# Performance work log

Hardware: AMD Instinct MI355X
Metric: run time of the kernel (lower is better)

## Reference

```python
import jax, jax.numpy as jnp
import numpy as np

N_NODES = 65536


def gcn_conv(x, W, b, src, dst, n_nodes):
    """PyG GCNConv: symmetric-normalized aggregation with self-loops.
    out = D^{-1/2} (A + I) D^{-1/2} (x W) + b, deg counted on targets incl. self-loop.
    """
    h = x @ W  # [N, F_out]
    # in-degree including the self-loop
    deg = jnp.zeros((n_nodes,), dtype=x.dtype).at[dst].add(1.0) + 1.0
    dis = jax.lax.rsqrt(deg)  # deg^{-1/2}
    norm = dis[src] * dis[dst]  # [E]
    msg = h[src] * norm[:, None]  # [E, F_out] gathered+scaled messages
    agg = jax.ops.segment_sum(msg, dst, num_segments=n_nodes)
    agg = agg + h * (dis * dis)[:, None]  # self-loop contribution, norm = dis[i]^2
    return agg + b


def setup_inputs() -> dict:
    key = jax.random.key(0)
    k1, k2, k3, k4 = jax.random.split(key, 4)
    d_in, d_hid = 64, 64
    x = jax.random.normal(k1, (N_NODES, d_in), dtype=jnp.float32)
    edge_index = jax.random.randint(k2, (2, 1048576), 0, N_NODES, dtype=jnp.int64)
    s = 1.0 / np.sqrt(d_in)
    W1 = jax.random.normal(k3, (d_in, d_hid), dtype=jnp.float32) * s
    b1 = jnp.zeros((d_hid,), dtype=jnp.float32)
    W2 = jax.random.normal(k4, (d_hid, d_hid), dtype=jnp.float32) * s
    b2 = jnp.zeros((d_hid,), dtype=jnp.float32)
    return {"x": x, "edge_index": edge_index, "W1": W1, "b1": b1, "W2": W2, "b2": b2}


def reference(x, edge_index, W1, b1, W2, b2):
    src, dst = edge_index[0], edge_index[1]
    n = x.shape[0]
    h = jax.nn.relu(gcn_conv(x, W1, b1, src, dst, n))
    h = jax.nn.relu(gcn_conv(h, W2, b2, src, dst, n))
    return h
```

## Files before the change

kernel.cpp:

```cpp
#include <hip/hip_runtime.h>

#define FDIM 64
#define EPB  2048
#define BCAP 6144

typedef float nf4 __attribute__((ext_vector_type(4)));
typedef float nf2 __attribute__((ext_vector_type(2)));

__device__ __forceinline__ unsigned f2bf(float f) {
    unsigned u = __float_as_uint(f);
    u += 0x7fffu + ((u >> 16) & 1u);
    return u >> 16;
}
__device__ __forceinline__ float bflo(unsigned u) { return __uint_as_float(u << 16); }
__device__ __forceinline__ float bfhi(unsigned u) { return __uint_as_float(u & 0xffff0000u); }


__global__ __launch_bounds__(256) void k_coarse(const int* __restrict__ ei,
                                                int* __restrict__ cursorG,
                                                int* __restrict__ packed, int nE) {
    __shared__ int lh[256], gb[256], lc[256];
    int t = threadIdx.x;
    lh[t] = 0; lc[t] = 0;
    __syncthreads();
    int base = blockIdx.x * EPB;
    int bins[EPB / 256], vals[EPB / 256];
    #pragma unroll
    for (int i = 0; i < EPB / 256; ++i) {
        int e = base + i * 256 + t;
        if (e < nE) {
            int s = ei[e];
            int d = ei[nE + e];
            bins[i] = d >> 8;
            vals[i] = (s << 8) | (d & 255);
            atomicAdd(&lh[bins[i]], 1);
        } else {
            bins[i] = -1;
        }
    }
    __syncthreads();
    gb[t] = atomicAdd(&cursorG[t], lh[t]);
    __syncthreads();
    #pragma unroll
    for (int i = 0; i < EPB / 256; ++i) {
        int b = bins[i];
        if (b >= 0) {
            int p = gb[b] + atomicAdd(&lc[b], 1);
            if (p < BCAP) packed[b * BCAP + p] = vals[i];
        }
    }
}


__global__ __launch_bounds__(256) void k_fine(const int* __restrict__ packed,
                                              const int* __restrict__ cursorG,
                                              float* __restrict__ dis,
                                              int* __restrict__ rowStart,
                                              unsigned short* __restrict__ lenArr,
                                              unsigned short* __restrict__ sortedSrc,
                                              int n) {
    __shared__ int cnt[256], loc[256], lc[256];
    int t = threadIdx.x;
    int b = blockIdx.x;
    int lo = b * BCAP;
    int hi = lo + cursorG[b];
    cnt[t] = 0; lc[t] = 0;
    __syncthreads();
    for (int k = lo + t; k < hi; k += 256)
        atomicAdd(&cnt[packed[k] & 255], 1);
    __syncthreads();

    int c = cnt[t];
    int node = (b << 8) + t;
    dis[node]    = rsqrtf((float)c + 1.0f);
    lenArr[node] = (unsigned short)c;

    loc[t] = c;
    __syncthreads();
    #pragma unroll
    for (int off = 1; off < 256; off <<= 1) {
        int u = (t >= off) ? loc[t - off] : 0;
        __syncthreads();
        loc[t] += u;
        __syncthreads();
    }
    int excl = loc[t] - c;
    rowStart[node] = lo + excl;
    __syncthreads();
    loc[t] = excl;
    __syncthreads();

    for (int k = lo + t; k < hi; k += 256) {
        int v = packed[k];
        int dl = v & 255;
        int p = loc[dl] + atomicAdd(&lc[dl], 1);
        sortedSrc[lo + p] = (unsigned short)(v >> 8);
    }
}


__global__ __launch_bounds__(256) void k_gemm64s(const float* __restrict__ X,
                                                 const float* __restrict__ W,
                                                 const float* __restrict__ dis,
                                                 unsigned* __restrict__ Hb) {
    __shared__ float Ws[64 * 64];
    __shared__ float XsT[64 * 68];

    const int tid  = threadIdx.x;
    const int row0 = blockIdx.x * 64;

    for (int i = tid; i < 4096; i += 256) Ws[i] = W[i];
    for (int i = tid; i < 4096; i += 256) {
        int r = i >> 6, k = i & 63;
        XsT[k * 68 + r] = X[(row0 + r) * FDIM + k];
    }
    __syncthreads();

    const int tx = tid & 15;
    const int ty = tid >> 4;

    float4 acc0 = {0,0,0,0}, acc1 = {0,0,0,0}, acc2 = {0,0,0,0}, acc3 = {0,0,0,0};

    #pragma unroll
    for (int k = 0; k < 64; ++k) {
        float4 wv = *(const float4*)&Ws[k * 64 + tx * 4];
        float4 xv = *(const float4*)&XsT[k * 68 + ty * 4];
        acc0.x = fmaf(xv.x, wv.x, acc0.x); acc0.y = fmaf(xv.x, wv.y, acc0.y);
        acc0.z = fmaf(xv.x, wv.z, acc0.z); acc0.w = fmaf(xv.x, wv.w, acc0.w);
        acc1.x = fmaf(xv.y, wv.x, acc1.x); acc1.y = fmaf(xv.y, wv.y, acc1.y);
        acc1.z = fmaf(xv.y, wv.z, acc1.z); acc1.w = fmaf(xv.y, wv.w, acc1.w);
        acc2.x = fmaf(xv.z, wv.x, acc2.x); acc2.y = fmaf(xv.z, wv.y, acc2.y);
        acc2.z = fmaf(xv.z, wv.z, acc2.z); acc2.w = fmaf(xv.z, wv.w, acc2.w);
        acc3.x = fmaf(xv.w, wv.x, acc3.x); acc3.y = fmaf(xv.w, wv.y, acc3.y);
        acc3.z = fmaf(xv.w, wv.z, acc3.z); acc3.w = fmaf(xv.w, wv.w, acc3.w);
    }

    float d0 = dis[row0 + ty * 4 + 0];
    float d1 = dis[row0 + ty * 4 + 1];
    float d2 = dis[row0 + ty * 4 + 2];
    float d3 = dis[row0 + ty * 4 + 3];

    uint2* H2 = (uint2*)Hb;
    uint2 o;
    o.x = f2bf(acc0.x * d0) | (f2bf(acc0.y * d0) << 16);
    o.y = f2bf(acc0.z * d0) | (f2bf(acc0.w * d0) << 16);
    H2[(row0 + ty * 4 + 0) * 16 + tx] = o;
    o.x = f2bf(acc1.x * d1) | (f2bf(acc1.y * d1) << 16);
    o.y = f2bf(acc1.z * d1) | (f2bf(acc1.w * d1) << 16);
    H2[(row0 + ty * 4 + 1) * 16 + tx] = o;
    o.x = f2bf(acc2.x * d2) | (f2bf(acc2.y * d2) << 16);
    o.y = f2bf(acc2.z * d2) | (f2bf(acc2.w * d2) << 16);
    H2[(row0 + ty * 4 + 2) * 16 + tx] = o;
    o.x = f2bf(acc3.x * d3) | (f2bf(acc3.y * d3) << 16);
    o.y = f2bf(acc3.z * d3) | (f2bf(acc3.w * d3) << 16);
    H2[(row0 + ty * 4 + 3) * 16 + tx] = o;
}


__global__ __launch_bounds__(256) void k_agg(const unsigned* __restrict__ Hb,
                                             const float* __restrict__ dis,
                                             const int* __restrict__ rowStart,
                                             const unsigned short* __restrict__ lenArr,
                                             const unsigned short* __restrict__ esrc,
                                             const float* __restrict__ bias,
                                             float* __restrict__ out) {
    const int tid = threadIdx.x;
    const int fq  = tid & 7;
    const int row = blockIdx.x * 32 + (tid >> 3);

    const int start = rowStart[row];
    const int end   = start + (int)lenArr[row];

    const uint4* H = (const uint4*)Hb;

    nf2 p0 = {0, 0}, p1 = {0, 0}, p2 = {0, 0}, p3 = {0, 0};

    int k = start;
    for (; k + 4 <= end; k += 4) {
        int s0 = (int)__builtin_nontemporal_load(&esrc[k]);
        int s1 = (int)__builtin_nontemporal_load(&esrc[k + 1]);
        int s2 = (int)__builtin_nontemporal_load(&esrc[k + 2]);
        int s3 = (int)__builtin_nontemporal_load(&esrc[k + 3]);
        uint4 v0 = H[s0 * 8 + fq];
        uint4 v1 = H[s1 * 8 + fq];
        uint4 v2 = H[s2 * 8 + fq];
        uint4 v3 = H[s3 * 8 + fq];
        p0 += (nf2){bflo(v0.x), bfhi(v0.x)}; p1 += (nf2){bflo(v0.y), bfhi(v0.y)};
        p2 += (nf2){bflo(v0.z), bfhi(v0.z)}; p3 += (nf2){bflo(v0.w), bfhi(v0.w)};
        p0 += (nf2){bflo(v1.x), bfhi(v1.x)}; p1 += (nf2){bflo(v1.y), bfhi(v1.y)};
        p2 += (nf2){bflo(v1.z), bfhi(v1.z)}; p3 += (nf2){bflo(v1.w), bfhi(v1.w)};
        p0 += (nf2){bflo(v2.x), bfhi(v2.x)}; p1 += (nf2){bflo(v2.y), bfhi(v2.y)};
        p2 += (nf2){bflo(v2.z), bfhi(v2.z)}; p3 += (nf2){bflo(v2.w), bfhi(v2.w)};
        p0 += (nf2){bflo(v3.x), bfhi(v3.x)}; p1 += (nf2){bflo(v3.y), bfhi(v3.y)};
        p2 += (nf2){bflo(v3.z), bfhi(v3.z)}; p3 += (nf2){bflo(v3.w), bfhi(v3.w)};
    }
    for (; k < end; ++k) {
        int s0 = (int)__builtin_nontemporal_load(&esrc[k]);
        uint4 v0 = H[s0 * 8 + fq];
        p0 += (nf2){bflo(v0.x), bfhi(v0.x)}; p1 += (nf2){bflo(v0.y), bfhi(v0.y)};
        p2 += (nf2){bflo(v0.z), bfhi(v0.z)}; p3 += (nf2){bflo(v0.w), bfhi(v0.w)};
    }

    uint4 sv = H[row * 8 + fq];
    float ds = dis[row];
    const float4* b4 = (const float4*)bias;
    float4 b0 = b4[fq * 2];
    float4 b1 = b4[fq * 2 + 1];

    nf4 r0, r1;
    r0.x = fmaxf(fmaf(p0.x + bflo(sv.x), ds, b0.x), 0.f);
    r0.y = fmaxf(fmaf(p0.y + bfhi(sv.x), ds, b0.y), 0.f);
    r0.z = fmaxf(fmaf(p1.x + bflo(sv.y), ds, b0.z), 0.f);
    r0.w = fmaxf(fmaf(p1.y + bfhi(sv.y), ds, b0.w), 0.f);
    r1.x = fmaxf(fmaf(p2.x + bflo(sv.z), ds, b1.x), 0.f);
    r1.y = fmaxf(fmaf(p2.y + bfhi(sv.z), ds, b1.y), 0.f);
    r1.z = fmaxf(fmaf(p3.x + bflo(sv.w), ds, b1.z), 0.f);
    r1.w = fmaxf(fmaf(p3.y + bfhi(sv.w), ds, b1.w), 0.f);

    nf4* O = (nf4*)out;
    __builtin_nontemporal_store(r0, &O[row * 16 + fq * 2]);
    __builtin_nontemporal_store(r1, &O[row * 16 + fq * 2 + 1]);
}


extern "C" void kernel_launch(void* const* d_in, const int* in_sizes, int n_in,
                              void* d_out, int out_size, void* d_ws, size_t ws_size,
                              hipStream_t stream) {
    const float* x  = (const float*)d_in[0];
    const int*   ei = (const int*)d_in[1];
    const float* W1 = (const float*)d_in[2];
    const float* b1 = (const float*)d_in[3];
    const float* W2 = (const float*)d_in[4];
    const float* b2 = (const float*)d_in[5];

    const int N = in_sizes[0] / FDIM;
    const int E = in_sizes[1] / 2;

    char* ws = (char*)d_ws;
    float*          dis       = (float*)(ws);
    int*            rowStart  = (int*)  (ws + 262144);
    unsigned short* lenArr    = (unsigned short*)(ws + 524288);
    int*            cursorG   = (int*)  (ws + 655360);
    unsigned short* sortedSrc = (unsigned short*)(ws + 656384);
    char*           heap      = ws + 656384 + 3145728;
    int*            packed    = (int*)heap;
    unsigned*       HSb       = (unsigned*)heap;
    float*          B         = (float*)d_out;

    hipMemsetAsync(cursorG, 0, 256 * sizeof(int), stream);
    k_coarse<<<(E + EPB - 1) / EPB, 256, 0, stream>>>(ei, cursorG, packed, E);
    k_fine  <<<256, 256, 0, stream>>>(packed, cursorG, dis, rowStart, lenArr, sortedSrc, N);

    k_gemm64s<<<N / 64, 256, 0, stream>>>(x, W1, dis, HSb);
    k_agg    <<<N / 32, 256, 0, stream>>>(HSb, dis, rowStart, lenArr, sortedSrc, b1, B);

    k_gemm64s<<<N / 64, 256, 0, stream>>>(B, W2, dis, HSb);
    k_agg    <<<N / 32, 256, 0, stream>>>(HSb, dis, rowStart, lenArr, sortedSrc, b2, (float*)d_out);
}
```

Measured before the change: 124.0 us.

## Fuse layer-1 aggregation with layer-2 GEMM and halve coarse-bin edges per block

Adds a k_aggemm kernel that aggregates layer-1 messages for 64 rows, applies bias and ReLU into shared memory, and multiplies by W2 in the same block. It writes scaled bf16 H for layer 2 directly. This removes the fp32 intermediate round-trip through global memory and one kernel launch. It also halves EPB so k_coarse launches more blocks with fewer edges each, which adds more global cursor atomics. The fused kernel uses 64-row blocks instead of 32 for aggregation, so fewer blocks do the gather work.

```diff
diff --git a/kernel.cpp b/kernel.cpp
--- a/kernel.cpp
+++ b/kernel.cpp
@@ -1,7 +1,7 @@
 #include <hip/hip_runtime.h>
 
 #define FDIM 64
-#define EPB  2048
+#define EPB  1024
 #define BCAP 6144
 
 typedef float nf4 __attribute__((ext_vector_type(4)));
@@ -50,7 +50,6 @@
         }
     }
 }
-
 
 __global__ __launch_bounds__(256) void k_fine(const int* __restrict__ packed,
                                               const int* __restrict__ cursorG,
@@ -141,6 +140,118 @@
     float d3 = dis[row0 + ty * 4 + 3];
 
     uint2* H2 = (uint2*)Hb;
+    uint2 o;
+    o.x = f2bf(acc0.x * d0) | (f2bf(acc0.y * d0) << 16);
+    o.y = f2bf(acc0.z * d0) | (f2bf(acc0.w * d0) << 16);
+    H2[(row0 + ty * 4 + 0) * 16 + tx] = o;
+    o.x = f2bf(acc1.x * d1) | (f2bf(acc1.y * d1) << 16);
+    o.y = f2bf(acc1.z * d1) | (f2bf(acc1.w * d1) << 16);
+    H2[(row0 + ty * 4 + 1) * 16 + tx] = o;
+    o.x = f2bf(acc2.x * d2) | (f2bf(acc2.y * d2) << 16);
+    o.y = f2bf(acc2.z * d2) | (f2bf(acc2.w * d2) << 16);
+    H2[(row0 + ty * 4 + 2) * 16 + tx] = o;
+    o.x = f2bf(acc3.x * d3) | (f2bf(acc3.y * d3) << 16);
+    o.y = f2bf(acc3.z * d3) | (f2bf(acc3.w * d3) << 16);
+    H2[(row0 + ty * 4 + 3) * 16 + tx] = o;
+}
+
+
+__global__ __launch_bounds__(256) void k_aggemm(const unsigned* __restrict__ Hb1,
+                                                const float* __restrict__ dis,
+                                                const int* __restrict__ rowStart,
+                                                const unsigned short* __restrict__ lenArr,
+                                                const unsigned short* __restrict__ esrc,
+                                                const float* __restrict__ bias,
+                                                const float* __restrict__ W,
+                                                unsigned* __restrict__ Hb2) {
+    __shared__ float Ws[64 * 64];
+    __shared__ float XsT[64 * 68];
+
+    const int tid  = threadIdx.x;
+    const int row0 = blockIdx.x * 64;
+
+    for (int i = tid; i < 4096; i += 256) Ws[i] = W[i];
+
+    const int fq = tid & 7;
+    const int rr = tid >> 3;
+    const uint4* H = (const uint4*)Hb1;
+    const float4* b4 = (const float4*)bias;
+    const float4 bb0 = b4[fq * 2];
+    const float4 bb1 = b4[fq * 2 + 1];
+
+    #pragma unroll
+    for (int half = 0; half < 2; ++half) {
+        const int r   = rr + half * 32;
+        const int row = row0 + r;
+        const int start = rowStart[row];
+        const int end   = start + (int)lenArr[row];
+
+        nf2 p0 = {0, 0}, p1 = {0, 0}, p2 = {0, 0}, p3 = {0, 0};
+        int k = start;
+        for (; k + 4 <= end; k += 4) {
+            int s0 = (int)__builtin_nontemporal_load(&esrc[k]);
+            int s1 = (int)__builtin_nontemporal_load(&esrc[k + 1]);
+            int s2 = (int)__builtin_nontemporal_load(&esrc[k + 2]);
+            int s3 = (int)__builtin_nontemporal_load(&esrc[k + 3]);
+            uint4 v0 = H[s0 * 8 + fq];
+            uint4 v1 = H[s1 * 8 + fq];
+            uint4 v2 = H[s2 * 8 + fq];
+            uint4 v3 = H[s3 * 8 + fq];
+            p0 += (nf2){bflo(v0.x), bfhi(v0.x)}; p1 += (nf2){bflo(v0.y), bfhi(v0.y)};
+            p2 += (nf2){bflo(v0.z), bfhi(v0.z)}; p3 += (nf2){bflo(v0.w), bfhi(v0.w)};
+            p0 += (nf2){bflo(v1.x), bfhi(v1.x)}; p1 += (nf2){bflo(v1.y), bfhi(v1.y)};
+            p2 += (nf2){bflo(v1.z), bfhi(v1.z)}; p3 += (nf2){bflo(v1.w), bfhi(v1.w)};
+            p0 += (nf2){bflo(v2.x), bfhi(v2.x)}; p1 += (nf2){bflo(v2.y), bfhi(v2.y)};
+            p2 += (nf2){bflo(v2.z), bfhi(v2.z)}; p3 += (nf2){bflo(v2.w), bfhi(v2.w)};
+            p0 += (nf2){bflo(v3.x), bfhi(v3.x)}; p1 += (nf2){bflo(v3.y), bfhi(v3.y)};
+            p2 += (nf2){bflo(v3.z), bfhi(v3.z)}; p3 += (nf2){bflo(v3.w), bfhi(v3.w)};
+        }
+        for (; k < end; ++k) {
+            int s0 = (int)__builtin_nontemporal_load(&esrc[k]);
+            uint4 v0 = H[s0 * 8 + fq];
+            p0 += (nf2){bflo(v0.x), bfhi(v0.x)}; p1 += (nf2){bflo(v0.y), bfhi(v0.y)};
+            p2 += (nf2){bflo(v0.z), bfhi(v0.z)}; p3 += (nf2){bflo(v0.w), bfhi(v0.w)};
+        }
+
+        uint4 sv = H[row * 8 + fq];
+        float ds = dis[row];
+        float* col = &XsT[(fq * 8) * 68 + r];
+        col[0 * 68] = fmaxf(fmaf(p0.x + bflo(sv.x), ds, bb0.x), 0.f);
+        col[1 * 68] = fmaxf(fmaf(p0.y + bfhi(sv.x), ds, bb0.y), 0.f);
+        col[2 * 68] = fmaxf(fmaf(p1.x + bflo(sv.y), ds, bb0.z), 0.f);
+        col[3 * 68] = fmaxf(fmaf(p1.y + bfhi(sv.y), ds, bb0.w), 0.f);
+        col[4 * 68] = fmaxf(fmaf(p2.x + bflo(sv.z), ds, bb1.x), 0.f);
+        col[5 * 68] = fmaxf(fmaf(p2.y + bfhi(sv.z), ds, bb1.y), 0.f);
+        col[6 * 68] = fmaxf(fmaf(p3.x + bflo(sv.w), ds, bb1.z), 0.f);
+        col[7 * 68] = fmaxf(fmaf(p3.y + bfhi(sv.w), ds, bb1.w), 0.f);
+    }
+    __syncthreads();
+
+    const int tx = tid & 15;
+    const int ty = tid >> 4;
+
+    float4 acc0 = {0,0,0,0}, acc1 = {0,0,0,0}, acc2 = {0,0,0,0}, acc3 = {0,0,0,0};
+
+    #pragma unroll
+    for (int k = 0; k < 64; ++k) {
+        float4 wv = *(const float4*)&Ws[k * 64 + tx * 4];
+        float4 xv = *(const float4*)&XsT[k * 68 + ty * 4];
+        acc0.x = fmaf(xv.x, wv.x, acc0.x); acc0.y = fmaf(xv.x, wv.y, acc0.y);
+        acc0.z = fmaf(xv.x, wv.z, acc0.z); acc0.w = fmaf(xv.x, wv.w, acc0.w);
+        acc1.x = fmaf(xv.y, wv.x, acc1.x); acc1.y = fmaf(xv.y, wv.y, acc1.y);
+        acc1.z = fmaf(xv.y, wv.z, acc1.z); acc1.w = fmaf(xv.y, wv.w, acc1.w);
+        acc2.x = fmaf(xv.z, wv.x, acc2.x); acc2.y = fmaf(xv.z, wv.y, acc2.y);
+        acc2.z = fmaf(xv.z, wv.z, acc2.z); acc2.w = fmaf(xv.z, wv.w, acc2.w);
+        acc3.x = fmaf(xv.w, wv.x, acc3.x); acc3.y = fmaf(xv.w, wv.y, acc3.y);
+        acc3.z = fmaf(xv.w, wv.z, acc3.z); acc3.w = fmaf(xv.w, wv.w, acc3.w);
+    }
+
+    float d0 = dis[row0 + ty * 4 + 0];
+    float d1 = dis[row0 + ty * 4 + 1];
+    float d2 = dis[row0 + ty * 4 + 2];
+    float d3 = dis[row0 + ty * 4 + 3];
+
+    uint2* H2 = (uint2*)Hb2;
     uint2 o;
     o.x = f2bf(acc0.x * d0) | (f2bf(acc0.y * d0) << 16);
     o.y = f2bf(acc0.z * d0) | (f2bf(acc0.w * d0) << 16);
@@ -244,16 +355,14 @@
     unsigned short* sortedSrc = (unsigned short*)(ws + 656384);
     char*           heap      = ws + 656384 + 3145728;
     int*            packed    = (int*)heap;
-    unsigned*       HSb       = (unsigned*)heap;
-    float*          B         = (float*)d_out;
+    unsigned*       HSb1      = (unsigned*)heap;
+    unsigned*       HSb2      = (unsigned*)(heap + 8388608);
 
     hipMemsetAsync(cursorG, 0, 256 * sizeof(int), stream);
     k_coarse<<<(E + EPB - 1) / EPB, 256, 0, stream>>>(ei, cursorG, packed, E);
     k_fine  <<<256, 256, 0, stream>>>(packed, cursorG, dis, rowStart, lenArr, sortedSrc, N);
 
-    k_gemm64s<<<N / 64, 256, 0, stream>>>(x, W1, dis, HSb);
-    k_agg    <<<N / 32, 256, 0, stream>>>(HSb, dis, rowStart, lenArr, sortedSrc, b1, B);
-
-    k_gemm64s<<<N / 64, 256, 0, stream>>>(B, W2, dis, HSb);
-    k_agg    <<<N / 32, 256, 0, stream>>>(HSb, dis, rowStart, lenArr, sortedSrc, b2, (float*)d_out);
-}
+    k_gemm64s<<<N / 64, 256, 0, stream>>>(x, W1, dis, HSb1);
+    k_aggemm <<<N / 64, 256, 0, stream>>>(HSb1, dis, rowStart, lenArr, sortedSrc, b1, W2, HSb2);
+    k_agg    <<<N / 32, 256, 0, stream>>>(HSb2, dis, rowStart, lenArr, sortedSrc, b2, (float*)d_out);
+}
```

Result: faster. 118.0 us (-4.8%).
